# Kernel optimization log

Measured on AMD Instinct MI355X. Metric: run time of the kernel, lower is better.

The kernel has to match this reference:

```python
import jax, jax.numpy as jnp
import numpy as np

D_BERT, D_LSTM, T, B = 768, 512, 256, 32
H = D_LSTM // 2  # per-direction hidden
X = 10           # additive attention hidden width


def setup_inputs() -> dict:
    key = jax.random.key(0)
    ks = jax.random.split(key, 12)
    s = lambda fan: 1.0 / np.sqrt(fan)
    u = lambda k, shape, fan: jax.random.uniform(k, shape, jnp.float32, -s(fan), s(fan))
    return {
        "x": jax.random.normal(ks[0], (B, T, D_BERT), jnp.float32),
        "mask": jnp.ones((B, T), jnp.float32),
        # forward-direction LSTM params (torch gate order i,f,g,o)
        "Wih_f": u(ks[1], (4 * H, D_BERT), H),
        "Whh_f": u(ks[2], (4 * H, H), H),
        "b_f": u(ks[3], (4 * H,), H),  # b_ih + b_hh fused
        # backward-direction LSTM params
        "Wih_b": u(ks[4], (4 * H, D_BERT), H),
        "Whh_b": u(ks[5], (4 * H, H), H),
        "b_b": u(ks[6], (4 * H,), H),
        # attention MLP: fc1 [X, 2*D_LSTM] no bias, fc2 [1, X] no bias, fc3 [D_LSTM, 2*D_LSTM] + bias
        "W1": u(ks[7], (X, 2 * D_LSTM), 2 * D_LSTM),
        "W2": u(ks[8], (1, X), X),
        "W3": u(ks[9], (D_LSTM, 2 * D_LSTM), 2 * D_LSTM),
        "b3": u(ks[10], (D_LSTM,), 2 * D_LSTM),
    }


def _lstm_dir(x_btd, Wih, Whh, b):
    """Single-direction LSTM over [B,T,D]; returns hidden states [B,T,H]."""
    Bc = x_btd.shape[0]
    h0 = jnp.zeros((Bc, H), x_btd.dtype)
    c0 = jnp.zeros((Bc, H), x_btd.dtype)
    # precompute input projections for all timesteps: [T,B,4H]
    xz = jnp.einsum('btd,gd->tbg', x_btd, Wih) + b

    def step(carry, xzt):
        h, c = carry
        z = xzt + h @ Whh.T
        i, f, g, o = jnp.split(z, 4, axis=-1)
        i, f, o = jax.nn.sigmoid(i), jax.nn.sigmoid(f), jax.nn.sigmoid(o)
        c = f * c + i * jnp.tanh(g)
        h = o * jnp.tanh(c)
        return (h, c), h

    _, hs = jax.lax.scan(step, (h0, c0), xz)
    return jnp.swapaxes(hs, 0, 1)  # [B,T,H]


def reference(x, mask, Wih_f, Whh_f, b_f, Wih_b, Whh_b, b_b, W1, W2, W3, b3):
    # Bidirectional LSTM: forward + reversed backward pass, concat on features
    hf = _lstm_dir(x, Wih_f, Whh_f, b_f)
    hb = _lstm_dir(x[:, ::-1], Wih_b, Whh_b, b_b)[:, ::-1]
    h = jnp.concatenate([hf, hb], axis=-1)  # [B,T,D_LSTM]

    # Additive attention. fc1 has no bias, so fc1(cat(q,k)) = q@W1q.T + k@W1k.T;
    # compute per-token projections then broadcast-add -> only [B,T,T,X] materialized.
    W1q, W1k = W1[:, :D_LSTM], W1[:, D_LSTM:]
    sq = jnp.einsum('btd,xd->btx', h, W1q)  # query proj [B,T,X]
    sk = jnp.einsum('btd,xd->btx', h, W1k)  # key proj   [B,T,X]
    a = jnp.einsum('bqkx,x->bqk', jnp.tanh(sq[:, :, None, :] + sk[:, None, :, :]), W2[0])

    madd = jnp.where(mask == 0, -jnp.inf, 0.0)[:, None, :]  # [B,1,T]
    w = jax.nn.softmax(a + madd, axis=-1)                   # [B,T,T]
    context = jnp.einsum('bqk,bkd->bqd', w, h)              # [B,T,D_LSTM]

    y = jnp.concatenate([h, context], axis=-1) @ W3.T + b3  # [B,T,D_LSTM]
    return y
```

## Files before the change

kernel.cpp:

```cpp
#include <hip/hip_runtime.h>
#include <stdint.h>

#define B_   32
#define T_   256
#define H_   256
#define DB_  768
#define DL_  512

#define OFF_DTYPE 0u
#define OFF_XZ    69632u
#define XZ_DIR_ELEMS 8388608u
#define NEED_CONC (OFF_XZ + 2u*16777216u + 8388608u)
#define OFF_CTX   OFF_XZ
#define OFF_WATT  (OFF_XZ + 8388608u)
#define OFF_SQ    (OFF_XZ + 12582912u)
#define OFF_SK    (OFF_SQ + 327680u)

#define SENTINEL 0x7F7F7F7Fu

typedef __attribute__((ext_vector_type(8))) short bf16x8;
typedef __attribute__((ext_vector_type(4))) float f32x4;
typedef __attribute__((ext_vector_type(4))) uint32_t u32x4;
typedef unsigned short ushort_t;

__device__ __forceinline__ float b2f(ushort_t u){ union{float f; uint32_t i;} v; v.i=((uint32_t)u)<<16; return v.f; }
__device__ __forceinline__ ushort_t f2b(float f){
  union{float ff; uint32_t i;} v; v.ff=f;
  uint32_t r = v.i + 0x7fffu + ((v.i>>16)&1u);
  return (ushort_t)(r>>16);
}
__device__ __forceinline__ float sig_f(float x){ return 1.f/(1.f+__expf(-x)); }
__device__ __forceinline__ float tanh_f(float x){ return 1.f - 2.f/(1.f+__expf(2.f*x)); }

__device__ __forceinline__ bf16x8 load8(const ushort_t* p, size_t idx, int isbf){
  if (isbf) return *(const bf16x8*)(p + idx);
  const float* f = (const float*)p;
  bf16x8 r;
  #pragma unroll
  for (int i=0;i<8;++i) r[i] = (short)f2b(f[idx+i]);
  return r;
}
__device__ __forceinline__ float loadS(const ushort_t* p, size_t idx, int isbf){
  return isbf ? b2f(p[idx]) : ((const float*)p)[idx];
}

__global__ void detect_k(const uint32_t* __restrict__ x, char* __restrict__ ws){
  __shared__ int cnt;
  if (threadIdx.x == 0) cnt = 0;
  __syncthreads();
  int local = 0;
  #pragma unroll
  for (int i=0;i<4;++i){
    uint32_t w = x[threadIdx.x*4 + i];
    uint32_t lo = w & 0xFFFFu;
    int e = (int)((lo >> 7) & 0xFFu);
    if (e >= 118 && e <= 130) local++;
  }
  atomicAdd(&cnt, local);
  __syncthreads();
  if (threadIdx.x == 0) *(int*)(ws + OFF_DTYPE) = (cnt > 512) ? 1 : 0;
}

template<int MODE>
__global__ __launch_bounds__(256,2) void gemm_k(
    const ushort_t* __restrict__ A0, const ushort_t* __restrict__ A2,
    const ushort_t* __restrict__ Bm, const ushort_t* __restrict__ bias,
    ushort_t* __restrict__ Cout, char* __restrict__ ws,
    int lda, int ldb, int K, int dir, int aIn, int bIn,
    long aOffZ, long bOffZ, long cOffZ)
{
  __shared__ ushort_t As[8192];
  __shared__ ushort_t Bs[8192];
  const int dtf = *(const int*)(ws + OFF_DTYPE);
  const int aBF = aIn ? dtf : 1;
  const int bBF = bIn ? dtf : 1;
  const int tid = threadIdx.x;
  const int l  = tid & 63, wv = tid >> 6;
  const int lc = l & 15,  lh = l >> 4;
  const int m0 = blockIdx.x * 128, n0 = blockIdx.y * 128;
  const int z  = blockIdx.z;
  const ushort_t* Abase = A0 + (size_t)z * aOffZ;
  const ushort_t* Bbase = Bm + (size_t)z * bOffZ;
  const int srow = tid >> 3;
  const int sch  = tid & 7;

  f32x4 acc[4][4];
  #pragma unroll
  for (int i=0;i<4;++i)
    #pragma unroll
    for (int j=0;j<4;++j) acc[i][j] = (f32x4){0.f,0.f,0.f,0.f};

  bf16x8 ra[4], rb[4];
  #pragma unroll
  for (int p=0;p<4;++p){
    int row = p*32 + srow;
    int kk  = (sch ^ (row & 7)) * 8;
    ra[p] = load8(Abase, (size_t)(m0+row)*lda + kk, aBF);
    if (MODE==3){
      int q = p*256 + tid, kr = q>>4, c = q&15;
      rb[p] = load8(Bbase, (size_t)kr*ldb + n0 + c*8, 1);
    } else {
      rb[p] = load8(Bbase, (size_t)(n0+row)*ldb + kk, bBF);
    }
  }

  const int mo = (wv&1)*64, no = (wv>>1)*64;

  for (int k0 = 0; k0 < K; k0 += 64) {
    #pragma unroll
    for (int p=0;p<4;++p){
      int row = p*32 + srow;
      *(bf16x8*)(&As[row*64 + sch*8]) = ra[p];
      if (MODE==3){
        int q = p*256 + tid, kr = q>>4, c = q&15;
        *(bf16x8*)(&Bs[kr*128 + c*8]) = rb[p];
      } else {
        *(bf16x8*)(&Bs[row*64 + sch*8]) = rb[p];
      }
    }
    __syncthreads();
    int k1 = k0 + 64;
    if (k1 < K) {
      #pragma unroll
      for (int p=0;p<4;++p){
        int row = p*32 + srow;
        int kk  = k1 + (sch ^ (row & 7)) * 8;
        if (MODE==2 && k1 >= 512)
          ra[p] = load8(A2, (size_t)(m0+row)*512 + (kk - 512), 1);
        else
          ra[p] = load8(Abase, (size_t)(m0+row)*lda + kk, aBF);
        if (MODE==3){
          int q = p*256 + tid, kr = q>>4, c = q&15;
          rb[p] = load8(Bbase, (size_t)(k1+kr)*ldb + n0 + c*8, 1);
        } else {
          rb[p] = load8(Bbase, (size_t)(n0+row)*ldb + kk, bBF);
        }
      }
    }
    #pragma unroll
    for (int kc=0;kc<2;++kc){
      bf16x8 af[4], bfv[4];
      #pragma unroll
      for (int it=0;it<4;++it){
        int m = mo + it*16 + lc;
        int gc = kc*4 + lh;
        af[it]  = *(const bf16x8*)(&As[m*64 + ((gc ^ (m&7))*8)]);
        int n = no + it*16 + lc;
        if (MODE==3){
          #pragma unroll
          for (int j=0;j<8;++j) bfv[it][j] = (short)Bs[(kc*32 + lh*8 + j)*128 + n];
        } else {
          bfv[it] = *(const bf16x8*)(&Bs[n*64 + ((gc ^ (n&7))*8)]);
        }
      }
      #pragma unroll
      for (int mt=0;mt<4;++mt)
        #pragma unroll
        for (int nt=0;nt<4;++nt)
          acc[mt][nt] = __builtin_amdgcn_mfma_f32_16x16x32_bf16(af[mt], bfv[nt], acc[mt][nt], 0,0,0);
    }
    __syncthreads();
  }

  ushort_t* xzsw = (ushort_t*)(ws + OFF_XZ);
  #pragma unroll
  for (int mt=0;mt<4;++mt){
    #pragma unroll
    for (int nt=0;nt<4;++nt){
      #pragma unroll
      for (int r=0;r<4;++r){
        int m = m0 + mo + mt*16 + lh*4 + r;
        int n = n0 + no + nt*16 + lc;
        float v = acc[mt][nt][r];
        if (MODE==0){
          v += loadS(bias, n, bBF);
          int b = m >> 8, t = m & 255;
          int ts = dir ? (255 - t) : t;
          int q = n >> 8, jm = n & 255;
          int w = jm >> 6, jj = jm & 63, wvv = jj >> 4, colj = jj & 15;
          int lane = ((b >> 2) & 3)*16 + colj;
          int idx  = (b >> 4)*16 + q*4 + (b & 3);
          size_t e = (((size_t)(w*4 + wvv)*256 + ts)*2048) + (size_t)lane*32 + idx;
          xzsw[e + (size_t)cOffZ] = f2b(v);
        } else if (MODE==3){
          Cout[(size_t)z*cOffZ + (size_t)m*DL_ + n] = f2b(v);
        } else {
          v += loadS(bias, n, bBF);
          if (dtf) Cout[(size_t)m*DL_ + n] = f2b(v);
          else     ((float*)Cout)[(size_t)m*DL_ + n] = v;
        }
      }
    }
  }
}

__global__ __launch_bounds__(256,1) void rec_k(
    const ushort_t* __restrict__ Whh_f, const ushort_t* __restrict__ Whh_b,
    char* __restrict__ ws, ushort_t* __restrict__ hist,
    int dParam, long xzDirStride)
{
  __shared__ ushort_t wlds[32768];
  const int d  = (gridDim.x == 16) ? (int)(blockIdx.x >> 3) : dParam;
  const int bw = (int)(blockIdx.x & 7);
  const int tid = threadIdx.x;
  const int wv = tid >> 6, l = tid & 63;
  const int lc = l & 15, lh = l >> 4;
  const int bh = wv & 1, hh = wv >> 1;
  const int dtf = *(const int*)(ws + OFF_DTYPE);

  const ushort_t* xz = (const ushort_t*)(ws + OFF_XZ) + (size_t)d * xzDirStride;
  const ushort_t* Whh = d ? Whh_b : Whh_f;

  const int jj = bw*32 + hh*16 + lc;
  const int g  = bw*2 + hh;

  #pragma unroll
  for (int i=0;i<16;++i){
    int f   = wv*16 + i;
    int fhh = f >> 5, fnt = (f >> 3) & 3, fkc = f & 7;
    int row = fnt*256 + bw*32 + fhh*16 + lc;
    bf16x8 v = load8(Whh, (size_t)row*256 + fkc*32 + lh*8, dtf);
    *(bf16x8*)(&wlds[f*512 + l*8]) = v;
  }
  __syncthreads();
  const int wbase = (hh*4)*8;

  float cst[4] = {0.f, 0.f, 0.f, 0.f};

  const ushort_t* xzb = xz + (size_t)g*256*2048 + (size_t)l*32 + bh*16;
  const int bb = bh*16 + lc;
  const uint32_t hOffBase = (uint32_t)bb*262144u + (uint32_t)d*512u + (uint32_t)lh*16u;

  __amdgpu_buffer_rsrc_t hrs =
    __builtin_amdgcn_make_buffer_rsrc((void*)hist, (short)0, 0xFFFFFFFFu, 0x00020000);
  uint32_t* histw = (uint32_t*)hist;

  for (int t=0; t<T_; ++t){
    bf16x8 xzv[2];
    xzv[0] = *(const bf16x8*)(xzb + (size_t)t*2048);
    xzv[1] = *(const bf16x8*)(xzb + (size_t)t*2048 + 8);

    f32x4 acc[4];
    #pragma unroll
    for (int j=0;j<4;++j) acc[j] = (f32x4){0.f,0.f,0.f,0.f};

    if (t > 0){
      const int tsp = d ? (256 - t) : (t - 1);
      const uint32_t off0 = hOffBase + (uint32_t)tsp*1024u;
      u32x4 hreg[8];
      for (;;){
        asm volatile("" ::: "memory");
        #pragma unroll
        for (int kc=0;kc<8;++kc)
          hreg[kc] = __builtin_bit_cast(u32x4,
            __builtin_amdgcn_raw_buffer_load_b128(hrs, off0 + kc*64, 0, 17));
        int ok = 1;
        #pragma unroll
        for (int kc=0;kc<8;++kc){
          ok &= (hreg[kc][0] != SENTINEL);
          ok &= (hreg[kc][1] != SENTINEL);
          ok &= (hreg[kc][2] != SENTINEL);
          ok &= (hreg[kc][3] != SENTINEL);
        }
        if (__all(ok)) break;
      }
      asm volatile("" ::: "memory");

      #pragma unroll
      for (int kc=0;kc<8;++kc){
        bf16x8 a = __builtin_bit_cast(bf16x8, hreg[kc]);
        #pragma unroll
        for (int nt=0;nt<4;++nt){
          bf16x8 wfrag = *(const bf16x8*)(&wlds[(wbase + nt*8 + kc)*512 + l*8]);
          acc[nt] = __builtin_amdgcn_mfma_f32_16x16x32_bf16(a, wfrag, acc[nt], 0,0,0);
        }
      }
    }

    const int ts = d ? (255 - t) : t;
    #pragma unroll
    for (int r=0;r<4;++r){
      float zi = acc[0][r] + b2f((ushort_t)xzv[(r+0 )>>3][(r+0 )&7]);
      float zf = acc[1][r] + b2f((ushort_t)xzv[(r+4 )>>3][(r+4 )&7]);
      float zg = acc[2][r] + b2f((ushort_t)xzv[(r+8 )>>3][(r+8 )&7]);
      float zo = acc[3][r] + b2f((ushort_t)xzv[(r+12)>>3][(r+12)&7]);
      float ig = sig_f(zi), fg = sig_f(zf), gg = tanh_f(zg), og = sig_f(zo);
      float c = fg * cst[r] + ig * gg;
      cst[r] = c;
      float h = og * tanh_f(c);
      ushort_t h16 = f2b(h);
      uint32_t mine = (uint32_t)h16;
      uint32_t partner = (uint32_t)__shfl_xor((int)mine, 1);
      if ((lc & 1) == 0){
        int b = bh*16 + lh*4 + r;
        uint32_t packed = mine | (partner << 16);
        __hip_atomic_store(histw + (size_t)(b*256 + ts)*256 + (size_t)(d*128 + (jj>>1)),
                           packed, __ATOMIC_RELAXED, __HIP_MEMORY_SCOPE_AGENT);
      }
    }
  }
}

__global__ __launch_bounds__(256) void c1_k(char* __restrict__ ws, const ushort_t* __restrict__ W1,
                                            const ushort_t* __restrict__ hist)
{
  float* sq = (float*)(ws + OFF_SQ);
  float* sk = (float*)(ws + OFF_SK);
  const int dtf = *(const int*)(ws + OFF_DTYPE);
  int tid = threadIdx.x; int wv = tid>>6, l = tid&63;
  int row = blockIdx.x*4 + wv;
  bf16x8 hv = *(const bf16x8*)(hist + (size_t)row*512 + l*8);
  float hf[8];
  #pragma unroll
  for (int i=0;i<8;++i) hf[i] = b2f((ushort_t)hv[i]);
  #pragma unroll
  for (int x=0;x<10;++x){
    bf16x8 qv = load8(W1, (size_t)x*1024 + l*8, dtf);
    bf16x8 kv = load8(W1, (size_t)x*1024 + 512 + l*8, dtf);
    float pq=0.f, pk=0.f;
    #pragma unroll
    for (int i=0;i<8;++i){ pq += hf[i]*b2f((ushort_t)qv[i]); pk += hf[i]*b2f((ushort_t)kv[i]); }
    #pragma unroll
    for (int off=32; off>0; off>>=1){ pq += __shfl_xor(pq, off, 64); pk += __shfl_xor(pk, off, 64); }
    if (l == 0){ sq[row*10 + x] = pq; sk[row*10 + x] = pk; }
  }
}

__global__ __launch_bounds__(256) void c2_k(char* __restrict__ ws, const ushort_t* __restrict__ W2,
                                            const ushort_t* __restrict__ mask)
{
  const float* sq = (const float*)(ws + OFF_SQ);
  const float* sk = (const float*)(ws + OFF_SK);
  ushort_t* watt = (ushort_t*)(ws + OFF_WATT);
  const int dtf = *(const int*)(ws + OFF_DTYPE);
  int tid = threadIdx.x; int wv = tid>>6, l = tid&63;
  int bq = blockIdx.x*4 + wv;
  int b  = bq >> 8;
  float sqv[10], w2v[10];
  #pragma unroll
  for (int x=0;x<10;++x){ sqv[x] = sq[(size_t)bq*10+x]; w2v[x] = loadS(W2, x, dtf); }
  float a[4];
  #pragma unroll
  for (int kk=0;kk<4;++kk){
    int k = kk*64 + l;
    const float* skp = sk + ((size_t)b*256 + k)*10;
    float s = 0.f;
    #pragma unroll
    for (int x=0;x<10;++x) s += tanh_f(sqv[x] + skp[x]) * w2v[x];
    float mval = loadS(mask, (size_t)b*256 + k, dtf);
    a[kk] = (mval == 0.f) ? -1e30f : s;
  }
  float mx = fmaxf(fmaxf(a[0],a[1]), fmaxf(a[2],a[3]));
  #pragma unroll
  for (int off=32; off>0; off>>=1) mx = fmaxf(mx, __shfl_xor(mx, off, 64));
  float e[4], ssum=0.f;
  #pragma unroll
  for (int kk=0;kk<4;++kk){ e[kk] = __expf(a[kk]-mx); ssum += e[kk]; }
  #pragma unroll
  for (int off=32; off>0; off>>=1) ssum += __shfl_xor(ssum, off, 64);
  float inv = 1.f/ssum;
  #pragma unroll
  for (int kk=0;kk<4;++kk) watt[(size_t)bq*256 + kk*64 + l] = f2b(e[kk]*inv);
}

extern "C" void kernel_launch(void* const* d_in, const int* in_sizes, int n_in,
                              void* d_out, int out_size, void* d_ws, size_t ws_size,
                              hipStream_t stream)
{
  const ushort_t* x     = (const ushort_t*)d_in[0];
  const ushort_t* mask  = (const ushort_t*)d_in[1];
  const ushort_t* Wih_f = (const ushort_t*)d_in[2];
  const ushort_t* Whh_f = (const ushort_t*)d_in[3];
  const ushort_t* b_f   = (const ushort_t*)d_in[4];
  const ushort_t* Wih_b = (const ushort_t*)d_in[5];
  const ushort_t* Whh_b = (const ushort_t*)d_in[6];
  const ushort_t* b_b   = (const ushort_t*)d_in[7];
  const ushort_t* W1    = (const ushort_t*)d_in[8];
  const ushort_t* W2    = (const ushort_t*)d_in[9];
  const ushort_t* W3    = (const ushort_t*)d_in[10];
  const ushort_t* b3    = (const ushort_t*)d_in[11];
  ushort_t* out = (ushort_t*)d_out;
  char* ws = (char*)d_ws;

  const bool conc = ws_size >= (size_t)NEED_CONC;
  ushort_t* hist = (ushort_t*)(ws + OFF_XZ + (conc ? 33554432u : 16777216u));

  hipMemsetAsync(ws, 0, 4096, stream);
  hipMemsetAsync(hist, 0x7F, 8388608, stream);
  detect_k<<<dim3(1), dim3(256), 0, stream>>>((const uint32_t*)d_in[0], ws);

  dim3 blk(256);
  if (conc){
    gemm_k<0><<<dim3(64,8,1), blk, 0, stream>>>(x, nullptr, Wih_f, b_f, nullptr, ws,
                                                DB_, DB_, DB_, 0, 1, 1, 0,0, 0L);
    gemm_k<0><<<dim3(64,8,1), blk, 0, stream>>>(x, nullptr, Wih_b, b_b, nullptr, ws,
                                                DB_, DB_, DB_, 1, 1, 1, 0,0, (long)XZ_DIR_ELEMS);
    rec_k<<<dim3(16), blk, 0, stream>>>(Whh_f, Whh_b, ws, hist, 0, (long)XZ_DIR_ELEMS);
  } else {
    gemm_k<0><<<dim3(64,8,1), blk, 0, stream>>>(x, nullptr, Wih_f, b_f, nullptr, ws,
                                                DB_, DB_, DB_, 0, 1, 1, 0,0, 0L);
    rec_k<<<dim3(8), blk, 0, stream>>>(Whh_f, Whh_b, ws, hist, 0, 0L);
    gemm_k<0><<<dim3(64,8,1), blk, 0, stream>>>(x, nullptr, Wih_b, b_b, nullptr, ws,
                                                DB_, DB_, DB_, 1, 1, 1, 0,0, 0L);
    rec_k<<<dim3(8), blk, 0, stream>>>(Whh_f, Whh_b, ws, hist, 1, 0L);
  }
  c1_k<<<dim3(2048), blk, 0, stream>>>(ws, W1, hist);
  c2_k<<<dim3(2048), blk, 0, stream>>>(ws, W2, mask);
  gemm_k<3><<<dim3(2,4,32), blk, 0, stream>>>((ushort_t*)(ws+OFF_WATT), nullptr,
                                              hist, nullptr,
                                              (ushort_t*)(ws+OFF_CTX), ws,
                                              256, 512, 256, 0, 0, 0,
                                              65536L, 131072L, 131072L);
  gemm_k<2><<<dim3(64,4,1), blk, 0, stream>>>(hist, (ushort_t*)(ws+OFF_CTX),
                                              W3, b3, out, ws,
                                              512, 1024, 1024, 0, 0, 1, 0,0, 0L);
}
```

Before: 1.449 ms.

## Fuse forward and backward LSTM recurrences into one block per slice

Each recurrent block now holds both directions' Whh slices in LDS (128KB) and steps forward and backward alternately within one time loop. The grid drops from 16 to 8 blocks. One direction's MFMA and gate work can hide the latency of the other direction's spin-wait on the cross-block h exchange. The cost is twice the serial work per block, and the doubled LDS use could limit occupancy or fail to fit.

Result: slower. 1.526 ms (+5.3%).

```diff
diff --git a/kernel.cpp b/kernel.cpp
--- a/kernel.cpp
+++ b/kernel.cpp
@@ -194,13 +194,75 @@
   }
 }
 
+#define STEP_DIR(DD, CST, XZB, LBASE)                                              \
+  do {                                                                             \
+    bf16x8 xzv[2];                                                                 \
+    xzv[0] = *(const bf16x8*)((XZB) + (size_t)t*2048);                             \
+    xzv[1] = *(const bf16x8*)((XZB) + (size_t)t*2048 + 8);                         \
+    f32x4 acc[4];                                                                  \
+    _Pragma("unroll")                                                              \
+    for (int j=0;j<4;++j) acc[j] = (f32x4){0.f,0.f,0.f,0.f};                       \
+    if (t > 0){                                                                    \
+      const int tsp = (DD) ? (256 - t) : (t - 1);                                  \
+      const uint32_t off0 = (uint32_t)bb*262144u + (uint32_t)(DD)*512u             \
+                          + (uint32_t)lh*16u + (uint32_t)tsp*1024u;                \
+      u32x4 hreg[8];                                                               \
+      for (;;){                                                                    \
+        asm volatile("" ::: "memory");                                             \
+        _Pragma("unroll")                                                          \
+        for (int kc=0;kc<8;++kc)                                                   \
+          hreg[kc] = __builtin_bit_cast(u32x4,                                     \
+            __builtin_amdgcn_raw_buffer_load_b128(hrs, off0 + kc*64, 0, 17));      \
+        int ok = 1;                                                                \
+        _Pragma("unroll")                                                          \
+        for (int kc=0;kc<8;++kc){                                                  \
+          ok &= (hreg[kc][0] != SENTINEL);                                         \
+          ok &= (hreg[kc][1] != SENTINEL);                                         \
+          ok &= (hreg[kc][2] != SENTINEL);                                         \
+          ok &= (hreg[kc][3] != SENTINEL);                                         \
+        }                                                                          \
+        if (__all(ok)) break;                                                      \
+      }                                                                            \
+      asm volatile("" ::: "memory");                                               \
+      _Pragma("unroll")                                                            \
+      for (int kc=0;kc<8;++kc){                                                    \
+        bf16x8 a = __builtin_bit_cast(bf16x8, hreg[kc]);                           \
+        _Pragma("unroll")                                                          \
+        for (int nt=0;nt<4;++nt){                                                  \
+          bf16x8 wfrag = *(const bf16x8*)(&wlds[(LBASE) + (wbase + nt*8 + kc)*512 + l*8]); \
+          acc[nt] = __builtin_amdgcn_mfma_f32_16x16x32_bf16(a, wfrag, acc[nt], 0,0,0); \
+        }                                                                          \
+      }                                                                            \
+    }                                                                              \
+    const int ts = (DD) ? (255 - t) : t;                                           \
+    _Pragma("unroll")                                                              \
+    for (int r=0;r<4;++r){                                                         \
+      float zi = acc[0][r] + b2f((ushort_t)xzv[(r+0 )>>3][(r+0 )&7]);              \
+      float zf = acc[1][r] + b2f((ushort_t)xzv[(r+4 )>>3][(r+4 )&7]);              \
+      float zg = acc[2][r] + b2f((ushort_t)xzv[(r+8 )>>3][(r+8 )&7]);              \
+      float zo = acc[3][r] + b2f((ushort_t)xzv[(r+12)>>3][(r+12)&7]);              \
+      float ig = sig_f(zi), fg = sig_f(zf), gg = tanh_f(zg), og = sig_f(zo);       \
+      float c = fg * (CST)[r] + ig * gg;                                           \
+      (CST)[r] = c;                                                                \
+      float h = og * tanh_f(c);                                                    \
+      ushort_t h16 = f2b(h);                                                       \
+      uint32_t mine = (uint32_t)h16;                                               \
+      uint32_t partner = (uint32_t)__shfl_xor((int)mine, 1);                       \
+      if ((lc & 1) == 0){                                                          \
+        int b = bh*16 + lh*4 + r;                                                  \
+        uint32_t packed = mine | (partner << 16);                                  \
+        __hip_atomic_store(histw + (size_t)(b*256 + ts)*256 + (size_t)((DD)*128 + (jj>>1)), \
+                           packed, __ATOMIC_RELAXED, __HIP_MEMORY_SCOPE_AGENT);    \
+      }                                                                            \
+    }                                                                              \
+  } while(0)
+
 __global__ __launch_bounds__(256,1) void rec_k(
     const ushort_t* __restrict__ Whh_f, const ushort_t* __restrict__ Whh_b,
     char* __restrict__ ws, ushort_t* __restrict__ hist,
-    int dParam, long xzDirStride)
+    int dParam, long xzDirStride, int fused)
 {
-  __shared__ ushort_t wlds[32768];
-  const int d  = (gridDim.x == 16) ? (int)(blockIdx.x >> 3) : dParam;
+  __shared__ ushort_t wlds[65536];
   const int bw = (int)(blockIdx.x & 7);
   const int tid = threadIdx.x;
   const int wv = tid >> 6, l = tid & 63;
@@ -208,95 +270,45 @@
   const int bh = wv & 1, hh = wv >> 1;
   const int dtf = *(const int*)(ws + OFF_DTYPE);
 
-  const ushort_t* xz = (const ushort_t*)(ws + OFF_XZ) + (size_t)d * xzDirStride;
-  const ushort_t* Whh = d ? Whh_b : Whh_f;
-
   const int jj = bw*32 + hh*16 + lc;
   const int g  = bw*2 + hh;
 
-  #pragma unroll
-  for (int i=0;i<16;++i){
-    int f   = wv*16 + i;
-    int fhh = f >> 5, fnt = (f >> 3) & 3, fkc = f & 7;
-    int row = fnt*256 + bw*32 + fhh*16 + lc;
-    bf16x8 v = load8(Whh, (size_t)row*256 + fkc*32 + lh*8, dtf);
-    *(bf16x8*)(&wlds[f*512 + l*8]) = v;
+  const int nS = fused ? 2 : 1;
+  for (int s=0; s<nS; ++s){
+    const ushort_t* Whh = fused ? (s ? Whh_b : Whh_f) : (dParam ? Whh_b : Whh_f);
+    #pragma unroll
+    for (int i=0;i<16;++i){
+      int f   = wv*16 + i;
+      int fhh = f >> 5, fnt = (f >> 3) & 3, fkc = f & 7;
+      int row = fnt*256 + bw*32 + fhh*16 + lc;
+      bf16x8 v = load8(Whh, (size_t)row*256 + fkc*32 + lh*8, dtf);
+      *(bf16x8*)(&wlds[s*32768 + f*512 + l*8]) = v;
+    }
   }
   __syncthreads();
   const int wbase = (hh*4)*8;
-
-  float cst[4] = {0.f, 0.f, 0.f, 0.f};
-
-  const ushort_t* xzb = xz + (size_t)g*256*2048 + (size_t)l*32 + bh*16;
   const int bb = bh*16 + lc;
-  const uint32_t hOffBase = (uint32_t)bb*262144u + (uint32_t)d*512u + (uint32_t)lh*16u;
+
+  const ushort_t* xzbase = (const ushort_t*)(ws + OFF_XZ);
+  const ushort_t* xzb0 = xzbase + (fused ? 0 : 0) + (size_t)g*256*2048 + (size_t)l*32 + bh*16;
+  const ushort_t* xzb1 = xzbase + (size_t)xzDirStride + (size_t)g*256*2048 + (size_t)l*32 + bh*16;
 
   __amdgpu_buffer_rsrc_t hrs =
     __builtin_amdgcn_make_buffer_rsrc((void*)hist, (short)0, 0xFFFFFFFFu, 0x00020000);
   uint32_t* histw = (uint32_t*)hist;
 
-  for (int t=0; t<T_; ++t){
-    bf16x8 xzv[2];
-    xzv[0] = *(const bf16x8*)(xzb + (size_t)t*2048);
-    xzv[1] = *(const bf16x8*)(xzb + (size_t)t*2048 + 8);
-
-    f32x4 acc[4];
-    #pragma unroll
-    for (int j=0;j<4;++j) acc[j] = (f32x4){0.f,0.f,0.f,0.f};
-
-    if (t > 0){
-      const int tsp = d ? (256 - t) : (t - 1);
-      const uint32_t off0 = hOffBase + (uint32_t)tsp*1024u;
-      u32x4 hreg[8];
-      for (;;){
-        asm volatile("" ::: "memory");
-        #pragma unroll
-        for (int kc=0;kc<8;++kc)
-          hreg[kc] = __builtin_bit_cast(u32x4,
-            __builtin_amdgcn_raw_buffer_load_b128(hrs, off0 + kc*64, 0, 17));
-        int ok = 1;
-        #pragma unroll
-        for (int kc=0;kc<8;++kc){
-          ok &= (hreg[kc][0] != SENTINEL);
-          ok &= (hreg[kc][1] != SENTINEL);
-          ok &= (hreg[kc][2] != SENTINEL);
-          ok &= (hreg[kc][3] != SENTINEL);
-        }
-        if (__all(ok)) break;
-      }
-      asm volatile("" ::: "memory");
-
-      #pragma unroll
-      for (int kc=0;kc<8;++kc){
-        bf16x8 a = __builtin_bit_cast(bf16x8, hreg[kc]);
-        #pragma unroll
-        for (int nt=0;nt<4;++nt){
-          bf16x8 wfrag = *(const bf16x8*)(&wlds[(wbase + nt*8 + kc)*512 + l*8]);
-          acc[nt] = __builtin_amdgcn_mfma_f32_16x16x32_bf16(a, wfrag, acc[nt], 0,0,0);
-        }
-      }
-    }
-
-    const int ts = d ? (255 - t) : t;
-    #pragma unroll
-    for (int r=0;r<4;++r){
-      float zi = acc[0][r] + b2f((ushort_t)xzv[(r+0 )>>3][(r+0 )&7]);
-      float zf = acc[1][r] + b2f((ushort_t)xzv[(r+4 )>>3][(r+4 )&7]);
-      float zg = acc[2][r] + b2f((ushort_t)xzv[(r+8 )>>3][(r+8 )&7]);
-      float zo = acc[3][r] + b2f((ushort_t)xzv[(r+12)>>3][(r+12)&7]);
-      float ig = sig_f(zi), fg = sig_f(zf), gg = tanh_f(zg), og = sig_f(zo);
-      float c = fg * cst[r] + ig * gg;
-      cst[r] = c;
-      float h = og * tanh_f(c);
-      ushort_t h16 = f2b(h);
-      uint32_t mine = (uint32_t)h16;
-      uint32_t partner = (uint32_t)__shfl_xor((int)mine, 1);
-      if ((lc & 1) == 0){
-        int b = bh*16 + lh*4 + r;
-        uint32_t packed = mine | (partner << 16);
-        __hip_atomic_store(histw + (size_t)(b*256 + ts)*256 + (size_t)(d*128 + (jj>>1)),
-                           packed, __ATOMIC_RELAXED, __HIP_MEMORY_SCOPE_AGENT);
-      }
+  float cst0[4] = {0.f, 0.f, 0.f, 0.f};
+  float cst1[4] = {0.f, 0.f, 0.f, 0.f};
+
+  if (fused){
+    for (int t=0; t<T_; ++t){
+      STEP_DIR(0, cst0, xzb0, 0);
+      STEP_DIR(1, cst1, xzb1, 32768);
+    }
+  } else {
+    const int d = dParam;
+    for (int t=0; t<T_; ++t){
+      STEP_DIR(d, cst0, xzb0, 0);
     }
   }
 }
@@ -395,14 +407,14 @@
                                                 DB_, DB_, DB_, 0, 1, 1, 0,0, 0L);
     gemm_k<0><<<dim3(64,8,1), blk, 0, stream>>>(x, nullptr, Wih_b, b_b, nullptr, ws,
                                                 DB_, DB_, DB_, 1, 1, 1, 0,0, (long)XZ_DIR_ELEMS);
-    rec_k<<<dim3(16), blk, 0, stream>>>(Whh_f, Whh_b, ws, hist, 0, (long)XZ_DIR_ELEMS);
+    rec_k<<<dim3(8), blk, 0, stream>>>(Whh_f, Whh_b, ws, hist, 0, (long)XZ_DIR_ELEMS, 1);
   } else {
     gemm_k<0><<<dim3(64,8,1), blk, 0, stream>>>(x, nullptr, Wih_f, b_f, nullptr, ws,
                                                 DB_, DB_, DB_, 0, 1, 1, 0,0, 0L);
-    rec_k<<<dim3(8), blk, 0, stream>>>(Whh_f, Whh_b, ws, hist, 0, 0L);
+    rec_k<<<dim3(8), blk, 0, stream>>>(Whh_f, Whh_b, ws, hist, 0, 0L, 0);
     gemm_k<0><<<dim3(64,8,1), blk, 0, stream>>>(x, nullptr, Wih_b, b_b, nullptr, ws,
                                                 DB_, DB_, DB_, 1, 1, 1, 0,0, 0L);
-    rec_k<<<dim3(8), blk, 0, stream>>>(Whh_f, Whh_b, ws, hist, 1, 0L);
+    rec_k<<<dim3(8), blk, 0, stream>>>(Whh_f, Whh_b, ws, hist, 1, 0L, 0);
   }
   c1_k<<<dim3(2048), blk, 0, stream>>>(ws, W1, hist);
   c2_k<<<dim3(2048), blk, 0, stream>>>(ws, W2, mask);
```

## Keep each LSTM recurrence in one block per batch-half, dropping cross-block spin sync

Applied to the files above, without the earlier changes.

Replaces the 8-blocks-per-direction recurrence, which exchanged hidden states through global memory with sentinel spin-polling, with 2 blocks per direction. Each block owns 16 batch rows and the full hidden dimension, so h is shared through LDS with __syncthreads instead. Whh is split across registers (half), LDS (a quarter) and per-step global reloads (a quarter) to fit. The sentinel memset is removed. The cost is much less parallelism (4 CUs instead of 16), 4x more MFMA work per block per step, and repeated global weight loads each step.

Result: slower. 5.214 ms (+259.9%).

```diff
diff --git a/kernel.cpp b/kernel.cpp
--- a/kernel.cpp
+++ b/kernel.cpp
@@ -16,11 +16,8 @@
 #define OFF_SQ    (OFF_XZ + 12582912u)
 #define OFF_SK    (OFF_SQ + 327680u)
 
-#define SENTINEL 0x7F7F7F7Fu
-
 typedef __attribute__((ext_vector_type(8))) short bf16x8;
 typedef __attribute__((ext_vector_type(4))) float f32x4;
-typedef __attribute__((ext_vector_type(4))) uint32_t u32x4;
 typedef unsigned short ushort_t;
 
 __device__ __forceinline__ float b2f(ushort_t u){ union{float f; uint32_t i;} v; v.i=((uint32_t)u)<<16; return v.f; }
@@ -197,107 +194,140 @@
 __global__ __launch_bounds__(256,1) void rec_k(
     const ushort_t* __restrict__ Whh_f, const ushort_t* __restrict__ Whh_b,
     char* __restrict__ ws, ushort_t* __restrict__ hist,
-    int dParam, long xzDirStride)
+    int dParam, long xzDirStride, int concMode)
 {
-  __shared__ ushort_t wlds[32768];
-  const int d  = (gridDim.x == 16) ? (int)(blockIdx.x >> 3) : dParam;
-  const int bw = (int)(blockIdx.x & 7);
+  __shared__ ushort_t sm[69632];
+  const int bid = (int)blockIdx.x;
+  const int d  = concMode ? (bid >> 1) : dParam;
+  const int mh = bid & 1;
   const int tid = threadIdx.x;
-  const int wv = tid >> 6, l = tid & 63;
+  const int w = tid >> 6, l = tid & 63;
   const int lc = l & 15, lh = l >> 4;
-  const int bh = wv & 1, hh = wv >> 1;
   const int dtf = *(const int*)(ws + OFF_DTYPE);
 
   const ushort_t* xz = (const ushort_t*)(ws + OFF_XZ) + (size_t)d * xzDirStride;
   const ushort_t* Whh = d ? Whh_b : Whh_f;
 
-  const int jj = bw*32 + hh*16 + lc;
-  const int g  = bw*2 + hh;
-
-  #pragma unroll
-  for (int i=0;i<16;++i){
-    int f   = wv*16 + i;
-    int fhh = f >> 5, fnt = (f >> 3) & 3, fkc = f & 7;
-    int row = fnt*256 + bw*32 + fhh*16 + lc;
-    bf16x8 v = load8(Whh, (size_t)row*256 + fkc*32 + lh*8, dtf);
-    *(bf16x8*)(&wlds[f*512 + l*8]) = v;
+  bf16x8 wreg[64];
+  #pragma unroll
+  for (int kc=2;kc<8;++kc){
+    #pragma unroll
+    for (int gt=0;gt<4;++gt){
+      #pragma unroll
+      for (int nh=0;nh<4;++nh){
+        int row = gt*256 + w*64 + nh*16 + lc;
+        bf16x8 v = load8(Whh, (size_t)row*256 + kc*32 + lh*8, dtf);
+        if (kc < 4)
+          *(bf16x8*)(&sm[w*16384 + ((kc-2)*16 + gt*4 + nh)*512 + l*8]) = v;
+        else
+          wreg[(kc-4)*16 + gt*4 + nh] = v;
+      }
+    }
   }
   __syncthreads();
-  const int wbase = (hh*4)*8;
-
-  float cst[4] = {0.f, 0.f, 0.f, 0.f};
-
-  const ushort_t* xzb = xz + (size_t)g*256*2048 + (size_t)l*32 + bh*16;
-  const int bb = bh*16 + lc;
-  const uint32_t hOffBase = (uint32_t)bb*262144u + (uint32_t)d*512u + (uint32_t)lh*16u;
-
-  __amdgpu_buffer_rsrc_t hrs =
-    __builtin_amdgcn_make_buffer_rsrc((void*)hist, (short)0, 0xFFFFFFFFu, 0x00020000);
+
+  ushort_t* hs = &sm[65536];
   uint32_t* histw = (uint32_t*)hist;
 
+  float cst[16];
+  #pragma unroll
+  for (int i=0;i<16;++i) cst[i] = 0.f;
+
   for (int t=0; t<T_; ++t){
-    bf16x8 xzv[2];
-    xzv[0] = *(const bf16x8*)(xzb + (size_t)t*2048);
-    xzv[1] = *(const bf16x8*)(xzb + (size_t)t*2048 + 8);
-
-    f32x4 acc[4];
-    #pragma unroll
-    for (int j=0;j<4;++j) acc[j] = (f32x4){0.f,0.f,0.f,0.f};
+    const int ts = d ? (255 - t) : t;
+
+    bf16x8 xr[4][2];
+    #pragma unroll
+    for (int nh=0;nh<4;++nh){
+      size_t e = ((size_t)((w*4+nh)*256 + t))*2048 + (size_t)l*32 + (size_t)mh*16;
+      xr[nh][0] = *(const bf16x8*)(xz + e);
+      xr[nh][1] = *(const bf16x8*)(xz + e + 8);
+    }
+
+    f32x4 acc[4][4];
+    #pragma unroll
+    for (int gt=0;gt<4;++gt)
+      #pragma unroll
+      for (int nh=0;nh<4;++nh) acc[gt][nh] = (f32x4){0.f,0.f,0.f,0.f};
 
     if (t > 0){
-      const int tsp = d ? (256 - t) : (t - 1);
-      const uint32_t off0 = hOffBase + (uint32_t)tsp*1024u;
-      u32x4 hreg[8];
-      for (;;){
-        asm volatile("" ::: "memory");
-        #pragma unroll
-        for (int kc=0;kc<8;++kc)
-          hreg[kc] = __builtin_bit_cast(u32x4,
-            __builtin_amdgcn_raw_buffer_load_b128(hrs, off0 + kc*64, 0, 17));
-        int ok = 1;
-        #pragma unroll
-        for (int kc=0;kc<8;++kc){
-          ok &= (hreg[kc][0] != SENTINEL);
-          ok &= (hreg[kc][1] != SENTINEL);
-          ok &= (hreg[kc][2] != SENTINEL);
-          ok &= (hreg[kc][3] != SENTINEL);
+      bf16x8 s0[16];
+      #pragma unroll
+      for (int gt=0;gt<4;++gt)
+        #pragma unroll
+        for (int nh=0;nh<4;++nh)
+          s0[gt*4+nh] = load8(Whh, (size_t)(gt*256 + w*64 + nh*16 + lc)*256 + lh*8, dtf);
+
+      #pragma unroll
+      for (int kc=4;kc<8;++kc){
+        bf16x8 a = *(const bf16x8*)(&hs[lc*256 + kc*32 + lh*8]);
+        #pragma unroll
+        for (int gt=0;gt<4;++gt)
+          #pragma unroll
+          for (int nh=0;nh<4;++nh)
+            acc[gt][nh] = __builtin_amdgcn_mfma_f32_16x16x32_bf16(a, wreg[(kc-4)*16 + gt*4 + nh], acc[gt][nh], 0,0,0);
+      }
+      bf16x8 s1[16];
+      #pragma unroll
+      for (int gt=0;gt<4;++gt)
+        #pragma unroll
+        for (int nh=0;nh<4;++nh)
+          s1[gt*4+nh] = load8(Whh, (size_t)(gt*256 + w*64 + nh*16 + lc)*256 + 32 + lh*8, dtf);
+
+      #pragma unroll
+      for (int kc=2;kc<4;++kc){
+        bf16x8 a = *(const bf16x8*)(&hs[lc*256 + kc*32 + lh*8]);
+        #pragma unroll
+        for (int gt=0;gt<4;++gt)
+          #pragma unroll
+          for (int nh=0;nh<4;++nh){
+            bf16x8 bf = *(const bf16x8*)(&sm[w*16384 + ((kc-2)*16 + gt*4 + nh)*512 + l*8]);
+            acc[gt][nh] = __builtin_amdgcn_mfma_f32_16x16x32_bf16(a, bf, acc[gt][nh], 0,0,0);
+          }
+      }
+      {
+        bf16x8 a0 = *(const bf16x8*)(&hs[lc*256 + 0*32 + lh*8]);
+        #pragma unroll
+        for (int gt=0;gt<4;++gt)
+          #pragma unroll
+          for (int nh=0;nh<4;++nh)
+            acc[gt][nh] = __builtin_amdgcn_mfma_f32_16x16x32_bf16(a0, s0[gt*4+nh], acc[gt][nh], 0,0,0);
+        bf16x8 a1 = *(const bf16x8*)(&hs[lc*256 + 1*32 + lh*8]);
+        #pragma unroll
+        for (int gt=0;gt<4;++gt)
+          #pragma unroll
+          for (int nh=0;nh<4;++nh)
+            acc[gt][nh] = __builtin_amdgcn_mfma_f32_16x16x32_bf16(a1, s1[gt*4+nh], acc[gt][nh], 0,0,0);
+      }
+    }
+    __syncthreads();
+
+    #pragma unroll
+    for (int nh=0;nh<4;++nh){
+      #pragma unroll
+      for (int r=0;r<4;++r){
+        float zi = acc[0][nh][r] + b2f((ushort_t)xr[nh][0][r]);
+        float zf = acc[1][nh][r] + b2f((ushort_t)xr[nh][0][4+r]);
+        float zg = acc[2][nh][r] + b2f((ushort_t)xr[nh][1][r]);
+        float zo = acc[3][nh][r] + b2f((ushort_t)xr[nh][1][4+r]);
+        float ig = sig_f(zi), fg = sig_f(zf), gg = tanh_f(zg), og = sig_f(zo);
+        float c = fg * cst[nh*4+r] + ig * gg;
+        cst[nh*4+r] = c;
+        float h = og * tanh_f(c);
+        ushort_t h16 = f2b(h);
+        uint32_t mine = (uint32_t)h16;
+        uint32_t partner = (uint32_t)__shfl_xor((int)mine, 1);
+        if ((lc & 1) == 0){
+          uint32_t packed = mine | (partner << 16);
+          int u  = w*64 + nh*16 + lc;
+          int lb = lh*4 + r;
+          int gb = mh*16 + lb;
+          *(uint32_t*)(&hs[lb*256 + u]) = packed;
+          histw[(((size_t)(gb*256 + ts))*512 + (size_t)(d*256 + u)) >> 1] = packed;
         }
-        if (__all(ok)) break;
-      }
-      asm volatile("" ::: "memory");
-
-      #pragma unroll
-      for (int kc=0;kc<8;++kc){
-        bf16x8 a = __builtin_bit_cast(bf16x8, hreg[kc]);
-        #pragma unroll
-        for (int nt=0;nt<4;++nt){
-          bf16x8 wfrag = *(const bf16x8*)(&wlds[(wbase + nt*8 + kc)*512 + l*8]);
-          acc[nt] = __builtin_amdgcn_mfma_f32_16x16x32_bf16(a, wfrag, acc[nt], 0,0,0);
-        }
-      }
-    }
-
-    const int ts = d ? (255 - t) : t;
-    #pragma unroll
-    for (int r=0;r<4;++r){
-      float zi = acc[0][r] + b2f((ushort_t)xzv[(r+0 )>>3][(r+0 )&7]);
-      float zf = acc[1][r] + b2f((ushort_t)xzv[(r+4 )>>3][(r+4 )&7]);
-      float zg = acc[2][r] + b2f((ushort_t)xzv[(r+8 )>>3][(r+8 )&7]);
-      float zo = acc[3][r] + b2f((ushort_t)xzv[(r+12)>>3][(r+12)&7]);
-      float ig = sig_f(zi), fg = sig_f(zf), gg = tanh_f(zg), og = sig_f(zo);
-      float c = fg * cst[r] + ig * gg;
-      cst[r] = c;
-      float h = og * tanh_f(c);
-      ushort_t h16 = f2b(h);
-      uint32_t mine = (uint32_t)h16;
-      uint32_t partner = (uint32_t)__shfl_xor((int)mine, 1);
-      if ((lc & 1) == 0){
-        int b = bh*16 + lh*4 + r;
-        uint32_t packed = mine | (partner << 16);
-        __hip_atomic_store(histw + (size_t)(b*256 + ts)*256 + (size_t)(d*128 + (jj>>1)),
-                           packed, __ATOMIC_RELAXED, __HIP_MEMORY_SCOPE_AGENT);
-      }
-    }
+      }
+    }
+    __syncthreads();
   }
 }
 
@@ -386,7 +416,6 @@
   ushort_t* hist = (ushort_t*)(ws + OFF_XZ + (conc ? 33554432u : 16777216u));
 
   hipMemsetAsync(ws, 0, 4096, stream);
-  hipMemsetAsync(hist, 0x7F, 8388608, stream);
   detect_k<<<dim3(1), dim3(256), 0, stream>>>((const uint32_t*)d_in[0], ws);
 
   dim3 blk(256);
@@ -395,14 +424,14 @@
                                                 DB_, DB_, DB_, 0, 1, 1, 0,0, 0L);
     gemm_k<0><<<dim3(64,8,1), blk, 0, stream>>>(x, nullptr, Wih_b, b_b, nullptr, ws,
                                                 DB_, DB_, DB_, 1, 1, 1, 0,0, (long)XZ_DIR_ELEMS);
-    rec_k<<<dim3(16), blk, 0, stream>>>(Whh_f, Whh_b, ws, hist, 0, (long)XZ_DIR_ELEMS);
+    rec_k<<<dim3(4), blk, 0, stream>>>(Whh_f, Whh_b, ws, hist, 0, (long)XZ_DIR_ELEMS, 1);
   } else {
     gemm_k<0><<<dim3(64,8,1), blk, 0, stream>>>(x, nullptr, Wih_f, b_f, nullptr, ws,
                                                 DB_, DB_, DB_, 0, 1, 1, 0,0, 0L);
-    rec_k<<<dim3(8), blk, 0, stream>>>(Whh_f, Whh_b, ws, hist, 0, 0L);
+    rec_k<<<dim3(2), blk, 0, stream>>>(Whh_f, Whh_b, ws, hist, 0, 0L, 0);
     gemm_k<0><<<dim3(64,8,1), blk, 0, stream>>>(x, nullptr, Wih_b, b_b, nullptr, ws,
                                                 DB_, DB_, DB_, 1, 1, 1, 0,0, 0L);
-    rec_k<<<dim3(8), blk, 0, stream>>>(Whh_f, Whh_b, ws, hist, 1, 0L);
+    rec_k<<<dim3(2), blk, 0, stream>>>(Whh_f, Whh_b, ws, hist, 1, 0L, 0);
   }
   c1_k<<<dim3(2048), blk, 0, stream>>>(ws, W1, hist);
   c2_k<<<dim3(2048), blk, 0, stream>>>(ws, W2, mask);
```
